# Optimization experiments

Measured on AMD Instinct MI355X. Metric: run time of the kernel, lower is better.

## Reference

```python
import jax, jax.numpy as jnp
import numpy as np
from jax import lax

B, T_IN, T_AR = 512, 200, 200
H = 128
L = 2    # num_layers


def setup_inputs() -> dict:
    key = jax.random.key(0)
    k = jax.random.split(key, 8)
    s = 1.0 / np.sqrt(H)
    x = jax.random.normal(k[0], (B, T_IN, H), jnp.float32)
    lengths_in = jax.random.randint(k[1], (B,), T_IN // 2, T_IN + 1).astype(jnp.int32).at[0].set(T_IN)
    lengths_aureg = jax.random.randint(k[2], (B,), T_AR // 2, T_AR + 1).astype(jnp.int32).at[0].set(T_AR)
    mask_aureg = jnp.arange(T_AR)[None, :] < lengths_aureg[:, None]  # [B, T_ar] prefix mask
    W_ih = jax.random.uniform(k[3], (L, 4 * H, H), jnp.float32, -s, s)
    W_hh = jax.random.uniform(k[4], (L, 4 * H, H), jnp.float32, -s, s)
    b_ih = jax.random.uniform(k[5], (L, 4 * H), jnp.float32, -s, s)
    b_hh = jax.random.uniform(k[6], (L, 4 * H), jnp.float32, -s, s)
    return {"x": x, "lengths_in": lengths_in, "lengths_aureg": lengths_aureg,
            "mask_aureg": mask_aureg, "W_ih": W_ih, "W_hh": W_hh, "b_ih": b_ih, "b_hh": b_hh}


def _forward(x, lengths_in, mask_aureg, W_ih, W_hh, b_ih, b_hh):
    def cell_stack(x_t, h, c):
        # one LSTM time step through all layers. x_t: [B,H]; h,c: [L,B,H]
        inp = x_t
        hs, cs = [], []
        for l in range(L):
            z = inp @ W_ih[l].T + h[l] @ W_hh[l].T + (b_ih[l] + b_hh[l])
            i, f, g, o = jnp.split(z, 4, axis=-1)  # PyTorch gate order i,f,g,o
            c_new = jax.nn.sigmoid(f) * c[l] + jax.nn.sigmoid(i) * jnp.tanh(g)
            h_new = jax.nn.sigmoid(o) * jnp.tanh(c_new)
            hs.append(h_new)
            cs.append(c_new)
            inp = h_new
        return jnp.stack(hs), jnp.stack(cs)

    T_in = x.shape[1]
    mask_in = jnp.arange(T_in)[None, :] < lengths_in[:, None]  # [B, T_in]
    h0 = jnp.zeros((L, B, H), x.dtype)

    # Teacher-forcing pass == packed-sequence LSTM: states only advance where t < length,
    # padded output positions are zero (as pad_packed_sequence produces).
    def tf_step(carry, xs):
        h, c = carry
        x_t, m_t = xs  # [B,H], [B]
        h_new, c_new = cell_stack(x_t, h, c)
        m3 = m_t[None, :, None]
        h = jnp.where(m3, h_new, h)
        c = jnp.where(m3, c_new, c)
        out = jnp.where(m_t[:, None], h_new[-1], 0.0)
        return (h, c), out

    (h, c), outs_tf = lax.scan(tf_step, (h0, h0), (x.transpose(1, 0, 2), mask_in.T))
    outputs_teafo = outs_tf.transpose(1, 0, 2)  # [B, T_in, H]

    # input_aureg_init: last-layer hidden at each sequence's final real step
    x_init = h[-1]  # [B, H]

    def ar_step(carry, m_t):
        h, c, xp = carry
        h_new, c_new = cell_stack(xp, h, c)
        m3 = m_t[None, :, None]
        h = jnp.where(m3, h_new, h)
        c = jnp.where(m3, c_new, c)
        out = jnp.where(m_t[:, None], h_new[-1], 0.0)  # temp_output (zeros for inactive rows)
        return (h, c, out), out

    _, outs_ar = lax.scan(ar_step, (h, c, x_init), mask_aureg.T)
    outputs_aureg = outs_ar.transpose(1, 0, 2)  # [B, T_ar, H]
    return outputs_teafo, outputs_aureg


def reference(x, lengths_in, lengths_aureg, mask_aureg, W_ih, W_hh, b_ih, b_hh):
    return _forward(x, lengths_in, mask_aureg, W_ih, W_hh, b_ih, b_hh)
```

## Files before the change

### kernel.cpp

```cpp
#include <hip/hip_runtime.h>
#include <hip/hip_fp16.h>

typedef _Float16 half8 __attribute__((ext_vector_type(8)));
typedef _Float16 half4v __attribute__((ext_vector_type(4)));
typedef float f32x4 __attribute__((ext_vector_type(4)));

#define T_INS 200

constexpr int WI0O = 0;
constexpr int H0O  = 131072;
constexpr int H1O  = 139264;
constexpr int XTO  = 147456;
constexpr int BIO  = 155648;
constexpr int SMSZ = 159744;

constexpr size_t WSZ_PACK  = 524288;
constexpr size_t Z0_BYTES  = 209715200ull;
constexpr size_t WSZ_HOIST = WSZ_PACK + Z0_BYTES;

#define OFF(b, k) (((((b) << 8) | ((k) << 1))) ^ (((b) & 7) << 4))

#define BAR_K(n) asm volatile("s_waitcnt lgkmcnt(" #n ")\n\ts_barrier" ::: "memory")
#define SCHED_FENCE() __builtin_amdgcn_sched_barrier(0)

__device__ __forceinline__ float sigm(float x) {
  return __builtin_amdgcn_rcpf(1.0f + __builtin_amdgcn_exp2f(-1.44269504f * x));
}
__device__ __forceinline__ float tanh_f(float x) {
  return 1.0f - 2.0f * __builtin_amdgcn_rcpf(1.0f + __builtin_amdgcn_exp2f(2.88539008f * x));
}
__device__ __forceinline__ half8 cvt_frag(const float* __restrict__ src) {
  f32x4 a = *(const f32x4*)src;
  f32x4 b = *(const f32x4*)(src + 4);
  half8 h;
  h[0] = (_Float16)a[0]; h[1] = (_Float16)a[1]; h[2] = (_Float16)a[2]; h[3] = (_Float16)a[3];
  h[4] = (_Float16)b[0]; h[5] = (_Float16)b[1]; h[6] = (_Float16)b[2]; h[7] = (_Float16)b[3];
  return h;
}
__device__ __forceinline__ int perm_row8(int w, int mt, int r) {
  return (r & 3) * 128 + w * 16 + (r >> 2) * 4 + mt;
}

__global__ __launch_bounds__(256) void pack_kernel(const float* __restrict__ W_ih,
                                                   const float* __restrict__ W_hh,
                                                   char* __restrict__ ws) {
  int gid = blockIdx.x * 256 + threadIdx.x;
  int G = gid >> 6, lane = gid & 63;
  int region = G >> 7, F = G & 127;
  int w = F >> 4, mt = (F >> 2) & 3, kf = F & 3;
  int row = perm_row8(w, mt, lane & 15);
  int k0 = kf * 32 + (lane >> 4) * 8;
  const float* src;
  if (region == 0)      src = W_ih + (size_t)(512 + row) * 128 + k0;
  else if (region == 3) src = W_ih + (size_t)row * 128 + k0;
  else                  src = W_hh + (size_t)((region - 1) * 512 + row) * 128 + k0;
  *(half8*)(ws + (size_t)G * 1024 + lane * 16) = cvt_frag(src);
}

__global__ __launch_bounds__(512) void zgemm_kernel(const float* __restrict__ x,
                                                    const float* __restrict__ b_ih,
                                                    const float* __restrict__ b_hh,
                                                    char* __restrict__ ws) {
  __shared__ __attribute__((aligned(16))) char sx[4096];
  const int tid = threadIdx.x;
  const int w = tid >> 6, lane = tid & 63;
  const int lb = lane & 15, lg = lane >> 4;
  const int k0b = lg * 8;
  const int u0 = w * 16 + lg * 4;
  const int t = blockIdx.x >> 5, bg = blockIdx.x & 31;

  {
    int b = tid >> 5, k4 = (tid & 31) * 4;
    f32x4 v = *(const f32x4*)(x + ((size_t)(bg * 16 + b) * T_INS + t) * 128 + k4);
    half4v hx;
    hx[0] = (_Float16)v[0]; hx[1] = (_Float16)v[1];
    hx[2] = (_Float16)v[2]; hx[3] = (_Float16)v[3];
    *(half4v*)(sx + OFF(b, k4)) = hx;
  }
  __syncthreads();

  f32x4 acc[4];
#pragma unroll
  for (int mt = 0; mt < 4; ++mt)
#pragma unroll
    for (int q = 0; q < 4; ++q)
      acc[mt][q] = b_ih[q * 128 + u0 + mt] + b_hh[q * 128 + u0 + mt];

  half8 bf[4];
#pragma unroll
  for (int kf = 0; kf < 4; ++kf)
    bf[kf] = *(const half8*)(sx + OFF(lb, kf * 32 + k0b));

  const char* wbase = ws + 393216 + (size_t)lane * 16;
#pragma unroll
  for (int kf = 0; kf < 4; ++kf)
#pragma unroll
    for (int mt = 0; mt < 4; ++mt) {
      half8 a = *(const half8*)(wbase + (w * 16 + mt * 4 + kf) * 1024);
      acc[mt] = __builtin_amdgcn_mfma_f32_16x16x32_f16(a, bf[kf], acc[mt], 0, 0, 0);
    }

  char* zp = ws + WSZ_PACK + ((size_t)blockIdx.x * 8 + w) * 4096 + lane * 16;
#pragma unroll
  for (int mt = 0; mt < 4; ++mt)
    *(f32x4*)(zp + mt * 1024) = acc[mt];
}

template <int PACKED, int HOIST>
__global__ __launch_bounds__(512, 2) void lstm_kernel(
    const float* __restrict__ x, const int* __restrict__ len_in,
    const int* __restrict__ len_ar, const float* __restrict__ W_ih,
    const float* __restrict__ W_hh, const float* __restrict__ b_ih,
    const float* __restrict__ b_hh, const char* __restrict__ ws,
    float* __restrict__ out) {
  __shared__ __attribute__((aligned(16))) char sm[SMSZ];
  float* biasS = (float*)(sm + BIO);

  const int tid = threadIdx.x;
  const int w = tid >> 6, lane = tid & 63;
  const int lb = lane & 15, lg = lane >> 4;
  const int k0b = lg * 8;
  const int u0 = w * 16 + lg * 4;
  const int batch = blockIdx.x * 16 + lb;
  const int Lin = len_in[batch];
  const int Lar = len_ar[batch];

  for (int j = 0; j < 16; ++j) {
    int pos = tid * 256 + j * 16;
    int F = pos >> 10, ln = (pos >> 4) & 63;
    int fw = F >> 4, fmt = (F >> 2) & 3, fkf = F & 3;
    int row = perm_row8(fw, fmt, ln & 15);
    int k0 = fkf * 32 + (ln >> 4) * 8;
    *(half8*)(sm + WI0O + pos) = cvt_frag(W_ih + (size_t)row * 128 + k0);
  }
  for (int i = tid; i < 1024; i += 512) {
    int l = i >> 9, rp = i & 511, u = rp >> 2, q = rp & 3;
    biasS[i] = b_ih[l * 512 + q * 128 + u] + b_hh[l * 512 + q * 128 + u];
  }
#pragma unroll
  for (int i = 0; i < 2; ++i)
    *(f32x4*)(sm + H0O + tid * 16 + i * 8192) = (f32x4){0.f, 0.f, 0.f, 0.f};

  const int xb = tid >> 5, xk4 = (tid & 31) * 4;
  if (!HOIST) {
    f32x4 v = *(const f32x4*)(x + ((size_t)(blockIdx.x * 16 + xb) * T_INS) * 128 + xk4);
    half4v hx;
    hx[0] = (_Float16)v[0]; hx[1] = (_Float16)v[1];
    hx[2] = (_Float16)v[2]; hx[3] = (_Float16)v[3];
    *(half4v*)(sm + XTO + OFF(xb, xk4)) = hx;
  }

  half8 whh0[4][4], whh1[4][4], wi1[4][4];
  if (PACKED) {
    const char* base = ws + (size_t)lane * 16;
#pragma unroll
    for (int mt = 0; mt < 4; ++mt)
#pragma unroll
      for (int kf = 0; kf < 4; ++kf) {
        int fo = (w * 16 + mt * 4 + kf) * 1024;
        wi1[mt][kf]  = *(const half8*)(base + fo);
        whh0[mt][kf] = *(const half8*)(base + 131072 + fo);
        whh1[mt][kf] = *(const half8*)(base + 262144 + fo);
      }
  } else {
#pragma unroll
    for (int mt = 0; mt < 4; ++mt)
#pragma unroll
      for (int kf = 0; kf < 4; ++kf) {
        int row = perm_row8(w, mt, lb);
        wi1[mt][kf]  = cvt_frag(W_ih + (size_t)(512 + row) * 128 + kf * 32 + k0b);
        whh0[mt][kf] = cvt_frag(W_hh + (size_t)row * 128 + kf * 32 + k0b);
        whh1[mt][kf] = cvt_frag(W_hh + (size_t)(512 + row) * 128 + kf * 32 + k0b);
      }
  }

  float c0[4], c1[4];
  half4v hp0v, hp1v;
#pragma unroll
  for (int i = 0; i < 4; ++i) {
    c0[i] = c1[i] = 0.f;
    hp0v[i] = (_Float16)0.f; hp1v[i] = (_Float16)0.f;
  }
  __syncthreads();

  const float* xptr = x + ((size_t)(blockIdx.x * 16 + xb) * T_INS + 1) * 128 + xk4;
  float* optr = out + (size_t)batch * 25600 + u0;
  const size_t obase_ar = 13107200ull + (size_t)batch * 25600 + u0;
  const char* wi0base = sm + WI0O + w * 16384 + lane * 16;
  const char* zp = ws + WSZ_PACK + ((size_t)(blockIdx.x * 8 + w)) * 4096 + lane * 16;

  f32x4 acc[4];
  half8 bf[4];
  if (HOIST) {
#pragma unroll
    for (int mt = 0; mt < 4; ++mt) acc[mt] = *(const f32x4*)(zp + mt * 1024);
  } else {
#pragma unroll
    for (int mt = 0; mt < 4; ++mt) acc[mt] = *(const f32x4*)(biasS + (u0 + mt) * 4);
  }
#pragma unroll
  for (int kf = 0; kf < 4; ++kf)
    bf[kf] = *(const half8*)(sm + H0O + 4096 + OFF(lb, kf * 32 + k0b));

  for (int t = 0; t < 400; ++t) {
    const int p = t & 1;
    const bool tf = (t < 200);
    const bool mk = tf ? (t < Lin) : ((t - 200) < Lar);

    f32x4 xpre = (f32x4){0.f, 0.f, 0.f, 0.f};
    if (!HOIST && t < 199) { xpre = *(const f32x4*)xptr; xptr += 128; }

#pragma unroll
    for (int kf = 0; kf < 4; ++kf)
#pragma unroll
      for (int mt = 0; mt < 4; ++mt)
        acc[mt] = __builtin_amdgcn_mfma_f32_16x16x32_f16(whh0[mt][kf], bf[kf],
                                                         acc[mt], 0, 0, 0);
    if (!HOIST || !tf) {
      const char* sX = tf ? (sm + XTO + p * 4096) : (sm + H1O + p * 4096);
#pragma unroll
      for (int kf = 0; kf < 4; ++kf)
        bf[kf] = *(const half8*)(sX + OFF(lb, kf * 32 + k0b));
#pragma unroll
      for (int kf = 0; kf < 4; ++kf)
#pragma unroll
        for (int mt = 0; mt < 4; ++mt) {
          half8 a = *(const half8*)(wi0base + (mt * 4 + kf) * 1024);
          acc[mt] = __builtin_amdgcn_mfma_f32_16x16x32_f16(a, bf[kf], acc[mt], 0, 0, 0);
        }
    }
    {
      _Float16 h4[4];
#pragma unroll
      for (int mt = 0; mt < 4; ++mt) {
        float si = sigm(acc[mt][0]);
        float sf = sigm(acc[mt][1]);
        float tg = tanh_f(acc[mt][2]);
        float so = sigm(acc[mt][3]);
        float cn = sf * c0[mt] + si * tg;
        float hn = so * tanh_f(cn);
        c0[mt] = mk ? cn : c0[mt];
        h4[mt] = (_Float16)hn;
      }
      hp0v = mk ? *(half4v*)h4 : hp0v;
      *(half4v*)(sm + H0O + p * 4096 + OFF(lb, u0)) = hp0v;
    }
    SCHED_FENCE();
    if (tf) {
#pragma unroll
      for (int kf = 0; kf < 4; ++kf)
        bf[kf] = *(const half8*)(sm + H1O + p * 4096 + OFF(lb, kf * 32 + k0b));
    }
#pragma unroll
    for (int mt = 0; mt < 4; ++mt)
      acc[mt] = *(const f32x4*)(biasS + 512 + (u0 + mt) * 4);
    SCHED_FENCE();
    if (tf) BAR_K(8); else BAR_K(4);

    if (!HOIST && t < 199) {
      half4v hx;
      hx[0] = (_Float16)xpre[0]; hx[1] = (_Float16)xpre[1];
      hx[2] = (_Float16)xpre[2]; hx[3] = (_Float16)xpre[3];
      *(half4v*)(sm + XTO + (p ^ 1) * 4096 + OFF(xb, xk4)) = hx;
    }

#pragma unroll
    for (int kf = 0; kf < 4; ++kf)
#pragma unroll
      for (int mt = 0; mt < 4; ++mt)
        acc[mt] = __builtin_amdgcn_mfma_f32_16x16x32_f16(whh1[mt][kf], bf[kf],
                                                         acc[mt], 0, 0, 0);
#pragma unroll
    for (int kf = 0; kf < 4; ++kf)
      bf[kf] = *(const half8*)(sm + H0O + p * 4096 + OFF(lb, kf * 32 + k0b));
#pragma unroll
    for (int kf = 0; kf < 4; ++kf)
#pragma unroll
      for (int mt = 0; mt < 4; ++mt)
        acc[mt] = __builtin_amdgcn_mfma_f32_16x16x32_f16(wi1[mt][kf], bf[kf],
                                                         acc[mt], 0, 0, 0);
    {
      _Float16 h4[4];
      f32x4 vo;
#pragma unroll
      for (int mt = 0; mt < 4; ++mt) {
        float si = sigm(acc[mt][0]);
        float sf = sigm(acc[mt][1]);
        float tg = tanh_f(acc[mt][2]);
        float so = sigm(acc[mt][3]);
        float cn = sf * c1[mt] + si * tg;
        float hn = so * tanh_f(cn);
        c1[mt] = mk ? cn : c1[mt];
        h4[mt] = (_Float16)hn;
        vo[mt] = mk ? hn : 0.0f;
      }
      hp1v = mk ? *(half4v*)h4 : hp1v;
      *(half4v*)(sm + H1O + (p ^ 1) * 4096 + OFF(lb, u0)) = hp1v;
      *(f32x4*)optr = vo;
      optr += 128;
      if (t == 199) optr = out + obase_ar;
    }
    SCHED_FENCE();
    if (HOIST && t + 1 < 200) {
      zp += 1048576;
#pragma unroll
      for (int mt = 0; mt < 4; ++mt) acc[mt] = *(const f32x4*)(zp + mt * 1024);
      SCHED_FENCE();
      BAR_K(0);
    } else {
#pragma unroll
      for (int mt = 0; mt < 4; ++mt) acc[mt] = *(const f32x4*)(biasS + (u0 + mt) * 4);
      SCHED_FENCE();
      BAR_K(4);
    }
  }
}

extern "C" void kernel_launch(void* const* d_in, const int* in_sizes, int n_in,
                              void* d_out, int out_size, void* d_ws, size_t ws_size,
                              hipStream_t stream) {
  (void)in_sizes; (void)n_in; (void)out_size;
  const float* x = (const float*)d_in[0];
  const int* len_in = (const int*)d_in[1];
  const int* len_ar = (const int*)d_in[2];
  const float* W_ih = (const float*)d_in[4];
  const float* W_hh = (const float*)d_in[5];
  const float* b_ih = (const float*)d_in[6];
  const float* b_hh = (const float*)d_in[7];
  float* out = (float*)d_out;
  char* ws = (char*)d_ws;

  const bool packed = ws_size >= WSZ_PACK;
  const bool hoist  = ws_size >= WSZ_HOIST;

  if (packed) pack_kernel<<<dim3(128), dim3(256), 0, stream>>>(W_ih, W_hh, ws);
  if (hoist)  zgemm_kernel<<<dim3(6400), dim3(512), 0, stream>>>(x, b_ih, b_hh, ws);

  if (hoist)
    lstm_kernel<1, 1><<<dim3(32), dim3(512), 0, stream>>>(x, len_in, len_ar, W_ih,
                                                          W_hh, b_ih, b_hh, ws, out);
  else if (packed)
    lstm_kernel<1, 0><<<dim3(32), dim3(512), 0, stream>>>(x, len_in, len_ar, W_ih,
                                                          W_hh, b_ih, b_hh, ws, out);
  else
    lstm_kernel<0, 0><<<dim3(32), dim3(512), 0, stream>>>(x, len_in, len_ar, W_ih,
                                                          W_hh, b_ih, b_hh, ws, out);
}
```

Measured before the change: 1.305 ms.

## Prefetch hoisted input projections into an LDS ring via async global-to-LDS loads

The precomputed layer-0 input projections used to be loaded straight into registers at the end of each teacher-forcing step, which put the global-memory latency on the recurrent critical path. They are now issued two steps ahead with global_load_lds into a 3-slot LDS ring that reuses the W_ih region. The first-layer W_ih copy is therefore skipped during the teacher-forcing phase and reloaded from the workspace at step 200. The risks are the hand-tuned vmcnt waits, which must match the number of outstanding loads (output stores also count toward vmcnt), and LDS reuse races between waves.

```diff
diff --git a/kernel.cpp b/kernel.cpp
--- a/kernel.cpp
+++ b/kernel.cpp
@@ -22,6 +22,12 @@
 
 #define BAR_K(n) asm volatile("s_waitcnt lgkmcnt(" #n ")\n\ts_barrier" ::: "memory")
 #define SCHED_FENCE() __builtin_amdgcn_sched_barrier(0)
+
+__device__ __forceinline__ void gload_lds16(const char* g, char* l) {
+  __builtin_amdgcn_global_load_lds(
+      (const __attribute__((address_space(1))) unsigned int*)g,
+      (__attribute__((address_space(3))) unsigned int*)l, 16, 0, 0);
+}
 
 __device__ __forceinline__ float sigm(float x) {
   return __builtin_amdgcn_rcpf(1.0f + __builtin_amdgcn_exp2f(-1.44269504f * x));
@@ -125,13 +131,15 @@
   const int Lin = len_in[batch];
   const int Lar = len_ar[batch];
 
-  for (int j = 0; j < 16; ++j) {
-    int pos = tid * 256 + j * 16;
-    int F = pos >> 10, ln = (pos >> 4) & 63;
-    int fw = F >> 4, fmt = (F >> 2) & 3, fkf = F & 3;
-    int row = perm_row8(fw, fmt, ln & 15);
-    int k0 = fkf * 32 + (ln >> 4) * 8;
-    *(half8*)(sm + WI0O + pos) = cvt_frag(W_ih + (size_t)row * 128 + k0);
+  if (!HOIST) {
+    for (int j = 0; j < 16; ++j) {
+      int pos = tid * 256 + j * 16;
+      int F = pos >> 10, ln = (pos >> 4) & 63;
+      int fw = F >> 4, fmt = (F >> 2) & 3, fkf = F & 3;
+      int row = perm_row8(fw, fmt, ln & 15);
+      int k0 = fkf * 32 + (ln >> 4) * 8;
+      *(half8*)(sm + WI0O + pos) = cvt_frag(W_ih + (size_t)row * 128 + k0);
+    }
   }
   for (int i = tid; i < 1024; i += 512) {
     int l = i >> 9, rp = i & 511, u = rp >> 2, q = rp & 3;
@@ -187,13 +195,26 @@
   float* optr = out + (size_t)batch * 25600 + u0;
   const size_t obase_ar = 13107200ull + (size_t)batch * 25600 + u0;
   const char* wi0base = sm + WI0O + w * 16384 + lane * 16;
-  const char* zp = ws + WSZ_PACK + ((size_t)(blockIdx.x * 8 + w)) * 4096 + lane * 16;
+  char* ringw = sm + WI0O + w * 4096;
+
+  auto issueZ = [&](const char* g, int s) {
+#pragma unroll
+    for (int mt = 0; mt < 4; ++mt)
+      gload_lds16(g + mt * 1024, ringw + s * 32768 + mt * 1024);
+  };
 
   f32x4 acc[4];
   half8 bf[4];
+  const char* ziss = ws + WSZ_PACK + ((size_t)(blockIdx.x * 8 + w)) * 4096 + lane * 16;
+  int sIss = 2, sNxt = 1;
   if (HOIST) {
-#pragma unroll
-    for (int mt = 0; mt < 4; ++mt) acc[mt] = *(const f32x4*)(zp + mt * 1024);
+    issueZ(ziss, 0);
+    issueZ(ziss + (1 << 20), 1);
+    ziss += (2 << 20);
+    asm volatile("s_waitcnt vmcnt(4)" ::: "memory");
+#pragma unroll
+    for (int mt = 0; mt < 4; ++mt)
+      acc[mt] = *(const f32x4*)(ringw + mt * 1024 + lane * 16);
   } else {
 #pragma unroll
     for (int mt = 0; mt < 4; ++mt) acc[mt] = *(const f32x4*)(biasS + (u0 + mt) * 4);
@@ -206,6 +227,19 @@
     const int p = t & 1;
     const bool tf = (t < 200);
     const bool mk = tf ? (t < Lin) : ((t - 200) < Lar);
+
+    if (HOIST && tf && t < 198) {
+      issueZ(ziss, sIss);
+      ziss += (1 << 20);
+      sIss = (sIss >= 2) ? 0 : sIss + 1;
+    }
+    if (HOIST && t == 200) {
+      const char* wsrc = ws + 393216 + (size_t)w * 16384 + lane * 16;
+#pragma unroll
+      for (int j = 0; j < 16; ++j)
+        gload_lds16(wsrc + j * 1024, sm + WI0O + w * 16384 + j * 1024);
+      asm volatile("s_waitcnt vmcnt(0)" ::: "memory");
+    }
 
     f32x4 xpre = (f32x4){0.f, 0.f, 0.f, 0.f};
     if (!HOIST && t < 199) { xpre = *(const f32x4*)xptr; xptr += 128; }
@@ -302,9 +336,11 @@
     }
     SCHED_FENCE();
     if (HOIST && t + 1 < 200) {
-      zp += 1048576;
-#pragma unroll
-      for (int mt = 0; mt < 4; ++mt) acc[mt] = *(const f32x4*)(zp + mt * 1024);
+      asm volatile("s_waitcnt vmcnt(5)" ::: "memory");
+#pragma unroll
+      for (int mt = 0; mt < 4; ++mt)
+        acc[mt] = *(const f32x4*)(ringw + sNxt * 32768 + mt * 1024 + lane * 16);
+      sNxt = (sNxt >= 2) ? 0 : sNxt + 1;
       SCHED_FENCE();
       BAR_K(0);
     } else {
```

Result: slower. 1.380 ms (+5.7%).
